# Kernel optimization log

Hardware: AMD Instinct MI355X
Metric: run time of the kernel (lower is better)

Reference implementation:

```python
import jax, jax.numpy as jnp
import numpy as np
from jax import lax

N, R, W, H = 256, 32, 8, 6       # batch, n_rooms, room width/height
MX, MY = 72, 72                  # map grid
EMB = 6                          # room embedding width
CIN = 10 + EMB                   # conv input channels


def _boundaries(m):
    # m: [R, W, H] binary room masks -> [R, 4, W, H] (left, right, up, down edges)
    left = jnp.concatenate([m[:, :1, :], jnp.clip(m[:, 1:, :] - m[:, :-1, :], 0)], axis=1)
    right = jnp.concatenate([jnp.clip(m[:, :-1, :] - m[:, 1:, :], 0), m[:, -1:, :]], axis=1)
    up = jnp.concatenate([m[:, :, :1], jnp.clip(m[:, :, 1:] - m[:, :, :-1], 0)], axis=2)
    down = jnp.concatenate([jnp.clip(m[:, :, :-1] - m[:, :, 1:], 0), m[:, :, -1:]], axis=2)
    return jnp.stack([left, right, up, down], axis=1)


def setup_inputs() -> dict:
    key = jax.random.key(0)
    ks = jax.random.split(key, 12)
    room_map = (jax.random.uniform(ks[0], (R, W, H)) < 0.7).astype(jnp.float32)
    room_map = room_map.at[:, 0, 0].set(1.0)  # guarantee nonempty rooms
    doors = (jax.random.uniform(ks[1], (R, 4, W, H)) < 0.15).astype(jnp.float32) * room_map[:, None]
    room_tensor = jnp.concatenate([room_map[:, None], doors, _boundaries(room_map)], axis=1)  # [R,9,W,H]
    px = jax.random.randint(ks[2], (N, R), 0, MX - W)
    py = jax.random.randint(ks[3], (N, R), 0, MY - H)
    room_positions = jnp.stack([px, py], axis=-1).astype(jnp.int32)  # [N,R,2]

    def rn(k, shape, fan_in):
        return jax.random.normal(k, shape, jnp.float32) / np.float32(np.sqrt(fan_in))

    inp = dict(room_positions=room_positions, room_tensor=room_tensor)
    inp['room_embedding'] = jax.random.normal(ks[4], (R, EMB), jnp.float32)
    inp['w_conv1'] = rn(ks[5], (64, CIN, 5, 5), CIN * 25); inp['b_conv1'] = jnp.zeros((64,), jnp.float32)
    inp['w_conv2'] = rn(ks[6], (64, 64, 3, 3), 64 * 9);    inp['b_conv2'] = jnp.zeros((64,), jnp.float32)
    inp['w_conv3'] = rn(ks[7], (64, 64, 3, 3), 64 * 9);    inp['b_conv3'] = jnp.zeros((64,), jnp.float32)
    inp['w_room1'] = rn(ks[8], (128, 64), 64);   inp['b_room1'] = jnp.zeros((128,), jnp.float32)
    inp['w_room2'] = rn(ks[9], (128, 128), 128); inp['b_room2'] = jnp.zeros((128,), jnp.float32)
    inp['w_fc1'] = rn(ks[10], (256, 128), 128);  inp['b_fc1'] = jnp.zeros((256,), jnp.float32)
    inp['w_fc2'] = rn(ks[11], (256, 256), 256);  inp['b_fc2'] = jnp.zeros((256,), jnp.float32)
    return inp


def _conv2d_relu(x, w, b):
    pad = w.shape[-1] // 2
    y = lax.conv_general_dilated(x, w, (1, 1), [(pad, pad), (pad, pad)],
                                 dimension_numbers=('NCHW', 'OIHW', 'NCHW'))
    return jax.nn.relu(y + b[None, :, None, None])


def _forward(room_positions, room_tensor, room_embedding,
             w_conv1, b_conv1, w_conv2, b_conv2, w_conv3, b_conv3,
             w_room1, b_room1, w_room2, b_room2, w_fc1, b_fc1, w_fc2, b_fc2):
    room_map = room_tensor[:, 0]                      # [R,W,H]
    px = room_positions[..., 0]                       # [N,R]
    py = room_positions[..., 1]
    # ---- encode_map: scatter-add all rooms into grid ----
    bidx = jnp.arange(N)[:, None, None, None, None]
    cidx = jnp.arange(9)[None, None, :, None, None]
    ix = px[:, :, None, None, None] + jnp.arange(W)[None, None, None, :, None]   # [N,R,1,W,1]
    iy = py[:, :, None, None, None] + jnp.arange(H)[None, None, None, None, :]   # [N,R,1,1,H]
    map9 = jnp.zeros((N, 9, MX, MY), jnp.float32).at[bidx, cidx, ix, iy].add(room_tensor[None])
    eidx = jnp.arange(EMB)[None, None, :, None, None]
    evals = room_embedding[:, :, None, None] * room_map[:, None, :, :]           # [R,EMB,W,H]
    embg = jnp.zeros((N, EMB, MX, MY), jnp.float32).at[bidx, eidx, ix, iy].add(evals[None])
    X = jnp.concatenate([map9, jnp.ones((N, 1, MX, MY), jnp.float32), embg], axis=1)  # [N,16,MX,MY]
    # ---- map convs ----
    X = _conv2d_relu(X, w_conv1, b_conv1)
    X = _conv2d_relu(X, w_conv2, b_conv2)
    X = _conv2d_relu(X, w_conv3, b_conv3)
    # ---- decode_map: gather room tiles, masked mean per room ----
    Xt = jnp.transpose(X, (0, 2, 3, 1))                                          # [N,MX,MY,C]
    g = Xt[jnp.arange(N)[:, None, None, None],
           px[:, :, None, None] + jnp.arange(W)[None, None, :, None],
           py[:, :, None, None] + jnp.arange(H)[None, None, None, :]]            # [N,R,W,H,C]
    g = g * room_map[None, :, :, :, None]
    room_feat = g.sum(axis=(2, 3)) / room_map.sum(axis=(1, 2))[None, :, None]    # [N,R,C]
    X = jnp.transpose(room_feat, (0, 2, 1))                                      # [N,C,R]
    # ---- 1x1 conv1d room layers ----
    X = jax.nn.relu(jnp.einsum('ncr,oc->nor', X, w_room1) + b_room1[None, :, None])
    X = jax.nn.relu(jnp.einsum('ncr,oc->nor', X, w_room2) + b_room2[None, :, None])
    # ---- fc head: sum over rooms, MLP ----
    X = X.sum(axis=2)                                                            # [N,128]
    X = jax.nn.relu(X @ w_fc1.T + b_fc1)
    return X @ w_fc2.T + b_fc2                                                   # [N,256]


def reference(room_positions, room_tensor, room_embedding,
              w_conv1, b_conv1, w_conv2, b_conv2, w_conv3, b_conv3,
              w_room1, b_room1, w_room2, b_room2, w_fc1, b_fc1, w_fc2, b_fc2):
    return _forward(room_positions, room_tensor, room_embedding,
                    w_conv1, b_conv1, w_conv2, b_conv2, w_conv3, b_conv3,
                    w_room1, b_room1, w_room2, b_room2, w_fc1, b_fc1, w_fc2, b_fc2)
```

## Files before the change

### kernel.cpp

```cpp
#include <hip/hip_runtime.h>
#include <hip/hip_bf16.h>
#include <cstddef>

#define NB 256
#define RR 32
#define WW 8
#define HH 6
#define MXY 72
#define EMB 6
#define CIN1 16

typedef __bf16 bf16x8 __attribute__((ext_vector_type(8)));
typedef float floatx4 __attribute__((ext_vector_type(4)));

static const size_t B_W1F  = 0;
static const size_t B_W2F  = 57344;
static const size_t B_W3F  = 131072;
static const size_t B_RAUX = 204800;
static const size_t B_RINV = 205056;
static const size_t B_HEAD = 205312;
static const size_t F_WR1T = 0;
static const size_t F_WR2T = 8192;
static const size_t F_F1T  = 24576;
static const size_t F_F2T  = 57344;
static const size_t B_FEAT = 696832;
static const size_t B_CHUNK = 2793984;
static const size_t PERN_BYTES = 165888;

__device__ inline short f2b(float f) {
    unsigned u = __builtin_bit_cast(unsigned, f);
    unsigned r = (u + 0x7fffu + ((u >> 16) & 1u)) >> 16;
    return (short)r;
}

__global__ void prep_weights(const float* __restrict__ w1, const float* __restrict__ w2,
                             const float* __restrict__ w3, const float* __restrict__ wr1,
                             const float* __restrict__ wr2, const float* __restrict__ wf1,
                             const float* __restrict__ wf2, char* __restrict__ ws)
{
    short* W1F = (short*)(ws + B_W1F);
    short* W2F = (short*)(ws + B_W2F);
    short* W3F = (short*)(ws + B_W3F);
    float* HEAD = (float*)(ws + B_HEAD);

    int idx = blockIdx.x * 256 + threadIdx.x;
    if (idx < 28672) {
        int j = idx & 7, lane = (idx >> 3) & 63, nt = (idx >> 9) & 3, kk = idx >> 11;
        int k = kk * 32 + (lane >> 4) * 8 + j;
        int oc = nt * 16 + (lane & 15);
        int tap = k >> 4, ci = k & 15;
        float v = (tap < 25) ? w1[(oc * 16 + ci) * 25 + tap] : 0.f;
        W1F[idx] = f2b(v);
        return;
    }
    idx -= 28672;
    if (idx < 36864) {
        int j = idx & 7, lane = (idx >> 3) & 63, nt = (idx >> 9) & 3, kk = idx >> 11;
        int k = kk * 32 + (lane >> 4) * 8 + j;
        int oc = nt * 16 + (lane & 15);
        int tap = k >> 6, cp = k & 63;
        int ci = (cp >> 2) + (cp & 3) * 16;
        W2F[idx] = f2b(w2[(oc * 64 + ci) * 9 + tap]);
        return;
    }
    idx -= 36864;
    if (idx < 36864) {
        int j = idx & 7, lane = (idx >> 3) & 63, nt = (idx >> 9) & 3, kk = idx >> 11;
        int k = kk * 32 + (lane >> 4) * 8 + j;
        int oc = nt * 16 + (lane & 15);
        int tap = k >> 6, cp = k & 63;
        int ci = (cp >> 2) + (cp & 3) * 16;
        W3F[idx] = f2b(w3[(oc * 64 + ci) * 9 + tap]);
        return;
    }
    idx -= 36864;
    if (idx < 8192)  { int o = idx & 127, c = idx >> 7; HEAD[F_WR1T + idx] = wr1[o * 64 + c]; return; }
    idx -= 8192;
    if (idx < 16384) { int o = idx & 127, c = idx >> 7; HEAD[F_WR2T + idx] = wr2[o * 128 + c]; return; }
    idx -= 16384;
    if (idx < 32768) { int o = idx & 255, c = idx >> 8; HEAD[F_F1T + idx] = wf1[o * 128 + c]; return; }
    idx -= 32768;
    if (idx < 65536) { int o = idx & 255, c = idx >> 8; HEAD[F_F2T + idx] = wf2[o * 256 + c]; return; }
}

__global__ void prep_rooms(const float* __restrict__ rt, char* __restrict__ ws)
{
    int r = threadIdx.x;
    if (r >= RR) return;
    unsigned long long m = 0ull;
    int cnt = 0;
    for (int j = 0; j < WW * HH; ++j)
        if (rt[r * 9 * 48 + j] != 0.f) { m |= (1ull << j); ++cnt; }
    ((unsigned long long*)(ws + B_RAUX))[r] = m;
    ((float*)(ws + B_RINV))[r] = 1.f / (float)cnt;
}

__global__ __launch_bounds__(256) void build_x(const int* __restrict__ pos,
                                               const float* __restrict__ rt,
                                               const float* __restrict__ emb,
                                               short* __restrict__ X, int n0)
{
    const int nl = blockIdx.y;
    const int n = n0 + nl;
    const int p = blockIdx.x * 256 + threadIdx.x;

    __shared__ int s_px[RR], s_py[RR];
    __shared__ float s_emb[RR * EMB];
    if (threadIdx.x < RR) {
        s_px[threadIdx.x] = pos[(n * RR + threadIdx.x) * 2 + 0];
        s_py[threadIdx.x] = pos[(n * RR + threadIdx.x) * 2 + 1];
    }
    for (int i = threadIdx.x; i < RR * EMB; i += 256) s_emb[i] = emb[i];
    __syncthreads();
    if (p >= MXY * MXY) return;

    const int gx = p / MXY, gy = p - (p / MXY) * MXY;

    float acc[16];
#pragma unroll
    for (int c = 0; c < 16; ++c) acc[c] = 0.f;
    acc[9] = 1.f;

    for (int r = 0; r < RR; ++r) {
        int w = gx - s_px[r], h = gy - s_py[r];
        if ((unsigned)w < (unsigned)WW && (unsigned)h < (unsigned)HH) {
            int j = w * HH + h;
            const float* rr = rt + r * 9 * 48;
#pragma unroll
            for (int c = 0; c < 9; ++c) acc[c] += rr[c * 48 + j];
            float m = rr[j];
#pragma unroll
            for (int e = 0; e < EMB; ++e) acc[10 + e] += s_emb[r * EMB + e] * m;
        }
    }

    short o[16];
#pragma unroll
    for (int c = 0; c < 16; ++c) o[c] = f2b(acc[c]);
    short* dst = X + ((size_t)nl * (MXY * MXY) + p) * CIN1;
    *reinterpret_cast<uint4*>(dst) = *reinterpret_cast<uint4*>(o);
    *reinterpret_cast<uint4*>(dst + 8) = *reinterpret_cast<uint4*>(o + 8);
}

__global__ __launch_bounds__(256, 4) void fused_conv(const short* __restrict__ X,
    const short* __restrict__ wAll, const float* __restrict__ bc1,
    const float* __restrict__ bc2, const float* __restrict__ bc3,
    const int* __restrict__ pos, const unsigned long long* __restrict__ rmask,
    float* __restrict__ feat, int n0)
{
    __shared__ __align__(16) short s_Y1[120 * 72];
    __shared__ __align__(16) short s_u[80 * 72];
    __shared__ float s_feat[64];

    const int tid = threadIdx.x;
    const int lane = tid & 63;
    const int wv = tid >> 6;
    const int ml = lane & 15;
    const int q = lane >> 4;
    const int room = blockIdx.x;
    const int nl = blockIdx.y;
    const int n = n0 + nl;

    const int px = pos[(n * RR + room) * 2 + 0];
    const int py = pos[(n * RR + room) * 2 + 1];

    const short* W1F = wAll;
    const short* W2F = wAll + B_W2F / 2;
    const short* W3F = wAll + B_W3F / 2;

    bf16x8 Bb[2][4];
    auto load_k = [&](const short* wF, int kk, bf16x8* dst) {
        const short* src = wF + (size_t)kk * 2048;
#pragma unroll
        for (int j2 = 0; j2 < 4; ++j2)
            dst[j2] = *reinterpret_cast<const bf16x8*>(src + (j2 * 64 + lane) * 8);
    };

    load_k(W1F, 0, Bb[0]);

    const short* Xn = X + (size_t)nl * (MXY * MXY) * CIN1;
    for (int i = tid; i < 448; i += 256) {
        int half = i & 1, pix = i >> 1;
        int row = pix / 14, col = pix - row * 14;
        int gx = px - 4 + row, gy = py - 4 + col;
        uint4 v = make_uint4(0u, 0u, 0u, 0u);
        if ((unsigned)gx < (unsigned)MXY && (unsigned)gy < (unsigned)MXY)
            v = *reinterpret_cast<const uint4*>(Xn + ((size_t)gx * MXY + gy) * CIN1 + half * 8);
        *reinterpret_cast<uint4*>(&s_u[pix * 24 + half * 8]) = v;
    }
    __syncthreads();

    {
        int prow[2], pcol[2];
#pragma unroll
        for (int i = 0; i < 2; ++i) {
            int p = wv * 32 + i * 16 + ml;
            if (p > 119) p = 119;
            prow[i] = p / 10; pcol[i] = p - prow[i] * 10;
        }
        floatx4 acc1[2][4] = {};

#pragma unroll
        for (int kk = 0; kk < 13; ++kk) {
            if (kk < 12) load_k(W1F, kk + 1, Bb[(kk + 1) & 1]);
            else         load_k(W2F, 0, Bb[1]);
            int tap = kk * 2 + (q >> 1);
            if (tap > 24) tap = 24;
            int chb = (q & 1) * 8;
            int dx = tap / 5, dy = tap - dx * 5;
            __builtin_amdgcn_s_setprio(1);
#pragma unroll
            for (int i = 0; i < 2; ++i) {
                bf16x8 A = *reinterpret_cast<const bf16x8*>(
                    &s_u[((prow[i] + dx) * 14 + (pcol[i] + dy)) * 24 + chb]);
#pragma unroll
                for (int j2 = 0; j2 < 4; ++j2)
                    acc1[i][j2] = __builtin_amdgcn_mfma_f32_16x16x32_bf16(
                        A, Bb[kk & 1][j2], acc1[i][j2], 0, 0, 0);
            }
            __builtin_amdgcn_s_setprio(0);
        }
        float b4[4];
#pragma unroll
        for (int j2 = 0; j2 < 4; ++j2) b4[j2] = bc1[j2 * 16 + ml];
#pragma unroll
        for (int i = 0; i < 2; ++i)
#pragma unroll
            for (int r = 0; r < 4; ++r) {
                int p = wv * 32 + i * 16 + q * 4 + r;
                if (p < 120) {
                    unsigned lo = (unsigned)(unsigned short)f2b(fmaxf(acc1[i][0][r] + b4[0], 0.f))
                                | ((unsigned)(unsigned short)f2b(fmaxf(acc1[i][1][r] + b4[1], 0.f)) << 16);
                    unsigned hi = (unsigned)(unsigned short)f2b(fmaxf(acc1[i][2][r] + b4[2], 0.f))
                                | ((unsigned)(unsigned short)f2b(fmaxf(acc1[i][3][r] + b4[3], 0.f)) << 16);
                    *reinterpret_cast<uint2*>(&s_Y1[p * 72 + ml * 4]) = make_uint2(lo, hi);
                }
            }
    }
    __syncthreads();

    {
        int prowA, pcolA, prowB, pcolB;
        {
            int p0 = wv * 16 + ml; prowA = p0 >> 3; pcolA = p0 & 7;
            int p1 = 64 + ml;      prowB = p1 >> 3; pcolB = p1 & 7;
        }
        floatx4 acc2[4] = {};
        floatx4 acc2s = {};

#pragma unroll
        for (int kk = 0; kk < 18; ++kk) {
            if (kk < 17) load_k(W2F, kk + 1, Bb[kk & 1]);
            else         load_k(W3F, 0, Bb[1]);
            bf16x8 B4 = *reinterpret_cast<const bf16x8*>(
                W2F + (size_t)kk * 2048 + (wv * 64 + lane) * 8);
            const int tap = kk >> 1;
            const int chb = (kk & 1) * 32 + q * 8;
            const int dx = tap / 3, dy = tap - (tap / 3) * 3;
            bf16x8 A0 = *reinterpret_cast<const bf16x8*>(
                &s_Y1[((prowA + dx) * 10 + (pcolA + dy)) * 72 + chb]);
            bf16x8 A4 = *reinterpret_cast<const bf16x8*>(
                &s_Y1[((prowB + dx) * 10 + (pcolB + dy)) * 72 + chb]);
            __builtin_amdgcn_s_setprio(1);
#pragma unroll
            for (int j2 = 0; j2 < 4; ++j2)
                acc2[j2] = __builtin_amdgcn_mfma_f32_16x16x32_bf16(A0, Bb[(kk + 1) & 1][j2], acc2[j2], 0, 0, 0);
            acc2s = __builtin_amdgcn_mfma_f32_16x16x32_bf16(A4, B4, acc2s, 0, 0, 0);
            __builtin_amdgcn_s_setprio(0);
        }
        float b4[4];
#pragma unroll
        for (int j2 = 0; j2 < 4; ++j2) b4[j2] = bc2[j2 * 16 + ml];
#pragma unroll
        for (int r = 0; r < 4; ++r) {
            int p = wv * 16 + q * 4 + r;
            unsigned lo = (unsigned)(unsigned short)f2b(fmaxf(acc2[0][r] + b4[0], 0.f))
                        | ((unsigned)(unsigned short)f2b(fmaxf(acc2[1][r] + b4[1], 0.f)) << 16);
            unsigned hi = (unsigned)(unsigned short)f2b(fmaxf(acc2[2][r] + b4[2], 0.f))
                        | ((unsigned)(unsigned short)f2b(fmaxf(acc2[3][r] + b4[3], 0.f)) << 16);
            *reinterpret_cast<uint2*>(&s_u[p * 72 + ml * 4]) = make_uint2(lo, hi);
        }
        {
            float bt = bc2[wv * 16 + ml];
#pragma unroll
            for (int r = 0; r < 4; ++r) {
                int p = 64 + q * 4 + r;
                s_u[p * 72 + ml * 4 + wv] = f2b(fmaxf(acc2s[r] + bt, 0.f));
            }
        }
        if (tid < 64) s_feat[tid] = 0.f;
    }
    __syncthreads();

    if (wv < 3) {
        int p0 = wv * 16 + ml;
        int row3 = p0 / 6, col3 = p0 - (p0 / 6) * 6;
        floatx4 acc3[4] = {};

#pragma unroll
        for (int kk = 0; kk < 18; ++kk) {
            if (kk < 17) load_k(W3F, kk + 1, Bb[kk & 1]);
            const int tap = kk >> 1;
            const int chb = (kk & 1) * 32 + q * 8;
            const int dx = tap / 3, dy = tap - (tap / 3) * 3;
            bf16x8 A = *reinterpret_cast<const bf16x8*>(
                &s_u[((row3 + dx) * 8 + (col3 + dy)) * 72 + chb]);
            __builtin_amdgcn_s_setprio(1);
#pragma unroll
            for (int j2 = 0; j2 < 4; ++j2)
                acc3[j2] = __builtin_amdgcn_mfma_f32_16x16x32_bf16(A, Bb[(kk + 1) & 1][j2], acc3[j2], 0, 0, 0);
            __builtin_amdgcn_s_setprio(0);
        }
        float b4[4];
#pragma unroll
        for (int j2 = 0; j2 < 4; ++j2) b4[j2] = bc3[j2 * 16 + ml];
        float part[4] = {0.f, 0.f, 0.f, 0.f};
        const unsigned long long mk = rmask[room];
#pragma unroll
        for (int r = 0; r < 4; ++r) {
            int p = wv * 16 + q * 4 + r;
            if ((mk >> p) & 1ull) {
#pragma unroll
                for (int j2 = 0; j2 < 4; ++j2)
                    part[j2] += fmaxf(acc3[j2][r] + b4[j2], 0.f);
            }
        }
#pragma unroll
        for (int j2 = 0; j2 < 4; ++j2) {
            part[j2] += __shfl_xor(part[j2], 16);
            part[j2] += __shfl_xor(part[j2], 32);
        }
        if (q == 0) {
#pragma unroll
            for (int j2 = 0; j2 < 4; ++j2)
                atomicAdd(&s_feat[j2 * 16 + ml], part[j2]);
        }
    }
    __syncthreads();
    if (tid < 64)
        feat[((size_t)n * RR + room) * 64 + tid] = s_feat[tid];
}

__global__ __launch_bounds__(256) void mlp_head(const float* __restrict__ feat,
                                                const float* __restrict__ HEAD,
                                                const float* __restrict__ rinv,
                                                const float* __restrict__ b1,
                                                const float* __restrict__ b2,
                                                const float* __restrict__ bf1,
                                                const float* __restrict__ bf2,
                                                float* __restrict__ outp)
{
    __shared__ __align__(16) float s_feat[RR * 64];
    __shared__ __align__(16) float s_h1[RR * 128];
    __shared__ __align__(16) float s_s[2 * 128];
    __shared__ __align__(16) float s_sf[128];
    __shared__ __align__(16) float s_t1[256];

    const int n = blockIdx.x;
    const int tid = threadIdx.x;
    const float* W1t = HEAD + F_WR1T;
    const float* W2t = HEAD + F_WR2T;
    const float* F1t = HEAD + F_F1T;
    const float* F2t = HEAD + F_F2T;

    for (int i = tid; i < RR * 64; i += 256)
        s_feat[i] = feat[(size_t)n * RR * 64 + i] * rinv[i >> 6];
    __syncthreads();

    const int o = tid & 127;
    const int rh = tid >> 7;

    float acc[16];
#pragma unroll
    for (int r = 0; r < 16; ++r) acc[r] = b1[o];
    for (int c4 = 0; c4 < 16; ++c4) {
        float w0 = W1t[(c4 * 4 + 0) * 128 + o];
        float w1 = W1t[(c4 * 4 + 1) * 128 + o];
        float w2 = W1t[(c4 * 4 + 2) * 128 + o];
        float w3 = W1t[(c4 * 4 + 3) * 128 + o];
#pragma unroll
        for (int r = 0; r < 16; ++r) {
            float4 f = *reinterpret_cast<const float4*>(&s_feat[(rh * 16 + r) * 64 + c4 * 4]);
            acc[r] += f.x * w0 + f.y * w1 + f.z * w2 + f.w * w3;
        }
    }
#pragma unroll
    for (int r = 0; r < 16; ++r) s_h1[(rh * 16 + r) * 128 + o] = fmaxf(acc[r], 0.f);
    __syncthreads();

#pragma unroll
    for (int r = 0; r < 16; ++r) acc[r] = b2[o];
    for (int c4 = 0; c4 < 32; ++c4) {
        float w0 = W2t[(c4 * 4 + 0) * 128 + o];
        float w1 = W2t[(c4 * 4 + 1) * 128 + o];
        float w2 = W2t[(c4 * 4 + 2) * 128 + o];
        float w3 = W2t[(c4 * 4 + 3) * 128 + o];
#pragma unroll
        for (int r = 0; r < 16; ++r) {
            float4 f = *reinterpret_cast<const float4*>(&s_h1[(rh * 16 + r) * 128 + c4 * 4]);
            acc[r] += f.x * w0 + f.y * w1 + f.z * w2 + f.w * w3;
        }
    }
    float ps = 0.f;
#pragma unroll
    for (int r = 0; r < 16; ++r) ps += fmaxf(acc[r], 0.f);
    s_s[rh * 128 + o] = ps;
    __syncthreads();
    if (tid < 128) s_sf[tid] = s_s[tid] + s_s[128 + tid];
    __syncthreads();

    {
        float a = bf1[tid];
        for (int c4 = 0; c4 < 32; ++c4) {
            float4 f = *reinterpret_cast<const float4*>(&s_sf[c4 * 4]);
            a += f.x * F1t[(c4 * 4 + 0) * 256 + tid];
            a += f.y * F1t[(c4 * 4 + 1) * 256 + tid];
            a += f.z * F1t[(c4 * 4 + 2) * 256 + tid];
            a += f.w * F1t[(c4 * 4 + 3) * 256 + tid];
        }
        s_t1[tid] = fmaxf(a, 0.f);
    }
    __syncthreads();

    {
        float a = bf2[tid];
        for (int c4 = 0; c4 < 64; ++c4) {
            float4 f = *reinterpret_cast<const float4*>(&s_t1[c4 * 4]);
            a += f.x * F2t[(c4 * 4 + 0) * 256 + tid];
            a += f.y * F2t[(c4 * 4 + 1) * 256 + tid];
            a += f.z * F2t[(c4 * 4 + 2) * 256 + tid];
            a += f.w * F2t[(c4 * 4 + 3) * 256 + tid];
        }
        outp[(size_t)n * 256 + tid] = a;
    }
}

extern "C" void kernel_launch(void* const* d_in, const int* in_sizes, int n_in,
                              void* d_out, int out_size, void* d_ws, size_t ws_size,
                              hipStream_t stream)
{
    const int* pos = (const int*)d_in[0];
    const float* rt = (const float*)d_in[1];
    const float* emb = (const float*)d_in[2];
    const float* w1 = (const float*)d_in[3];
    const float* bc1 = (const float*)d_in[4];
    const float* w2 = (const float*)d_in[5];
    const float* bc2 = (const float*)d_in[6];
    const float* w3 = (const float*)d_in[7];
    const float* bc3 = (const float*)d_in[8];
    const float* wr1 = (const float*)d_in[9];
    const float* br1 = (const float*)d_in[10];
    const float* wr2 = (const float*)d_in[11];
    const float* br2 = (const float*)d_in[12];
    const float* wf1 = (const float*)d_in[13];
    const float* bf1 = (const float*)d_in[14];
    const float* wf2 = (const float*)d_in[15];
    const float* bf2 = (const float*)d_in[16];
    float* out = (float*)d_out;
    char* ws = (char*)d_ws;

    prep_weights<<<880, 256, 0, stream>>>(w1, w2, w3, wr1, wr2, wf1, wf2, ws);
    prep_rooms<<<1, 64, 0, stream>>>(rt, ws);

    int nc = 16;
    const int cands[4] = {256, 128, 64, 32};
    for (int k = 0; k < 4; ++k) {
        size_t need = B_CHUNK + (size_t)cands[k] * PERN_BYTES;
        if (need <= ws_size) { nc = cands[k]; break; }
    }

    const short* WALL = (const short*)(ws + B_W1F);
    const unsigned long long* RMASK = (const unsigned long long*)(ws + B_RAUX);
    const float* RINV = (const float*)(ws + B_RINV);
    float* HEAD = (float*)(ws + B_HEAD);
    float* FEAT = (float*)(ws + B_FEAT);
    short* Xc = (short*)(ws + B_CHUNK);

    for (int n0 = 0; n0 < NB; n0 += nc) {
        build_x<<<dim3(21, nc), 256, 0, stream>>>(pos, rt, emb, Xc, n0);
        fused_conv<<<dim3(RR, nc), 256, 0, stream>>>(Xc, WALL, bc1, bc2, bc3,
                                                     pos, RMASK, FEAT, n0);
    }

    mlp_head<<<NB, 256, 0, stream>>>(FEAT, HEAD, RINV, br1, br2, bf1, bf2, out);
}
```

Baseline: 331.1 us.

## Fuse map construction into conv kernel using per-room overlap masks

Removes the separate build_x pass that rasterized the full 72x72x16 map for every batch element into a global buffer. Each conv block now builds only its own 14x16 patch, and a new prep kernel computes per-room bitmasks of nearby rooms so only candidate rooms are tested. The chunked batch loop is replaced by a single launch. This avoids the global write and read of the intermediate map at the cost of redundant rasterization in overlapping patches and uncoalesced global loads inside the conv kernel prologue.

```diff
diff --git a/kernel.cpp b/kernel.cpp
--- a/kernel.cpp
+++ b/kernel.cpp
@@ -24,8 +24,7 @@
 static const size_t F_F1T  = 24576;
 static const size_t F_F2T  = 57344;
 static const size_t B_FEAT = 696832;
-static const size_t B_CHUNK = 2793984;
-static const size_t PERN_BYTES = 165888;
+static const size_t B_IMSK = 2793984;
 
 __device__ inline short f2b(float f) {
     unsigned u = __builtin_bit_cast(unsigned, f);
@@ -95,58 +94,28 @@
     ((float*)(ws + B_RINV))[r] = 1.f / (float)cnt;
 }
 
-__global__ __launch_bounds__(256) void build_x(const int* __restrict__ pos,
-                                               const float* __restrict__ rt,
-                                               const float* __restrict__ emb,
-                                               short* __restrict__ X, int n0)
-{
-    const int nl = blockIdx.y;
-    const int n = n0 + nl;
-    const int p = blockIdx.x * 256 + threadIdx.x;
-
-    __shared__ int s_px[RR], s_py[RR];
-    __shared__ float s_emb[RR * EMB];
-    if (threadIdx.x < RR) {
-        s_px[threadIdx.x] = pos[(n * RR + threadIdx.x) * 2 + 0];
-        s_py[threadIdx.x] = pos[(n * RR + threadIdx.x) * 2 + 1];
-    }
-    for (int i = threadIdx.x; i < RR * EMB; i += 256) s_emb[i] = emb[i];
-    __syncthreads();
-    if (p >= MXY * MXY) return;
-
-    const int gx = p / MXY, gy = p - (p / MXY) * MXY;
-
-    float acc[16];
-#pragma unroll
-    for (int c = 0; c < 16; ++c) acc[c] = 0.f;
-    acc[9] = 1.f;
-
+__global__ void prep_imask(const int* __restrict__ pos, unsigned* __restrict__ imask)
+{
+    const int n = blockIdx.x;
+    const int r0 = threadIdx.x;
+    const int px0 = pos[(n * RR + r0) * 2 + 0];
+    const int py0 = pos[(n * RR + r0) * 2 + 1];
+    unsigned m = 0;
     for (int r = 0; r < RR; ++r) {
-        int w = gx - s_px[r], h = gy - s_py[r];
-        if ((unsigned)w < (unsigned)WW && (unsigned)h < (unsigned)HH) {
-            int j = w * HH + h;
-            const float* rr = rt + r * 9 * 48;
-#pragma unroll
-            for (int c = 0; c < 9; ++c) acc[c] += rr[c * 48 + j];
-            float m = rr[j];
-#pragma unroll
-            for (int e = 0; e < EMB; ++e) acc[10 + e] += s_emb[r * EMB + e] * m;
-        }
-    }
-
-    short o[16];
-#pragma unroll
-    for (int c = 0; c < 16; ++c) o[c] = f2b(acc[c]);
-    short* dst = X + ((size_t)nl * (MXY * MXY) + p) * CIN1;
-    *reinterpret_cast<uint4*>(dst) = *reinterpret_cast<uint4*>(o);
-    *reinterpret_cast<uint4*>(dst + 8) = *reinterpret_cast<uint4*>(o + 8);
-}
-
-__global__ __launch_bounds__(256, 4) void fused_conv(const short* __restrict__ X,
-    const short* __restrict__ wAll, const float* __restrict__ bc1,
-    const float* __restrict__ bc2, const float* __restrict__ bc3,
-    const int* __restrict__ pos, const unsigned long long* __restrict__ rmask,
-    float* __restrict__ feat, int n0)
+        int rpx = pos[(n * RR + r) * 2 + 0];
+        int rpy = pos[(n * RR + r) * 2 + 1];
+        if (rpx >= px0 - 11 && rpx <= px0 + 11 && rpy >= py0 - 9 && rpy <= py0 + 9)
+            m |= 1u << r;
+    }
+    imask[n * RR + r0] = m;
+}
+
+__global__ __launch_bounds__(256, 4) void fused_conv(
+    const unsigned* __restrict__ imask, const float* __restrict__ rt,
+    const float* __restrict__ emb, const short* __restrict__ wAll,
+    const float* __restrict__ bc1, const float* __restrict__ bc2,
+    const float* __restrict__ bc3, const int* __restrict__ pos,
+    const unsigned long long* __restrict__ rmask, float* __restrict__ feat)
 {
     __shared__ __align__(16) short s_Y1[120 * 72];
     __shared__ __align__(16) short s_u[80 * 72];
@@ -158,8 +127,7 @@
     const int ml = lane & 15;
     const int q = lane >> 4;
     const int room = blockIdx.x;
-    const int nl = blockIdx.y;
-    const int n = n0 + nl;
+    const int n = blockIdx.y;
 
     const int px = pos[(n * RR + room) * 2 + 0];
     const int py = pos[(n * RR + room) * 2 + 1];
@@ -178,15 +146,39 @@
 
     load_k(W1F, 0, Bb[0]);
 
-    const short* Xn = X + (size_t)nl * (MXY * MXY) * CIN1;
-    for (int i = tid; i < 448; i += 256) {
-        int half = i & 1, pix = i >> 1;
-        int row = pix / 14, col = pix - row * 14;
-        int gx = px - 4 + row, gy = py - 4 + col;
-        uint4 v = make_uint4(0u, 0u, 0u, 0u);
-        if ((unsigned)gx < (unsigned)MXY && (unsigned)gy < (unsigned)MXY)
-            v = *reinterpret_cast<const uint4*>(Xn + ((size_t)gx * MXY + gy) * CIN1 + half * 8);
-        *reinterpret_cast<uint4*>(&s_u[pix * 24 + half * 8]) = v;
+    {
+        const unsigned mk0 = imask[n * RR + room];
+        if (tid < 224) {
+            const int row = tid / 14, col = tid - (tid / 14) * 14;
+            const int gx = px - 4 + row, gy = py - 4 + col;
+            float a[16];
+#pragma unroll
+            for (int c = 0; c < 16; ++c) a[c] = 0.f;
+            a[9] = ((unsigned)gx < (unsigned)MXY && (unsigned)gy < (unsigned)MXY) ? 1.f : 0.f;
+
+            unsigned mm = mk0;
+            while (mm) {
+                const int r = __builtin_ctz(mm);
+                mm &= mm - 1;
+                const int rpx = pos[(n * RR + r) * 2 + 0];
+                const int rpy = pos[(n * RR + r) * 2 + 1];
+                const int w = gx - rpx, h = gy - rpy;
+                if ((unsigned)w < (unsigned)WW && (unsigned)h < (unsigned)HH) {
+                    const int j = w * HH + h;
+                    const float* rr = rt + r * 9 * 48;
+#pragma unroll
+                    for (int c = 0; c < 9; ++c) a[c] += rr[c * 48 + j];
+                    const float mv = rr[j];
+#pragma unroll
+                    for (int e = 0; e < EMB; ++e) a[10 + e] += emb[r * EMB + e] * mv;
+                }
+            }
+            short o[16];
+#pragma unroll
+            for (int c = 0; c < 16; ++c) o[c] = f2b(a[c]);
+            *reinterpret_cast<uint4*>(&s_u[tid * 24 + 0]) = *reinterpret_cast<uint4*>(o);
+            *reinterpret_cast<uint4*>(&s_u[tid * 24 + 8]) = *reinterpret_cast<uint4*>(o + 8);
+        }
     }
     __syncthreads();
 
@@ -462,25 +454,17 @@
     prep_weights<<<880, 256, 0, stream>>>(w1, w2, w3, wr1, wr2, wf1, wf2, ws);
     prep_rooms<<<1, 64, 0, stream>>>(rt, ws);
 
-    int nc = 16;
-    const int cands[4] = {256, 128, 64, 32};
-    for (int k = 0; k < 4; ++k) {
-        size_t need = B_CHUNK + (size_t)cands[k] * PERN_BYTES;
-        if (need <= ws_size) { nc = cands[k]; break; }
-    }
-
     const short* WALL = (const short*)(ws + B_W1F);
     const unsigned long long* RMASK = (const unsigned long long*)(ws + B_RAUX);
     const float* RINV = (const float*)(ws + B_RINV);
     float* HEAD = (float*)(ws + B_HEAD);
     float* FEAT = (float*)(ws + B_FEAT);
-    short* Xc = (short*)(ws + B_CHUNK);
-
-    for (int n0 = 0; n0 < NB; n0 += nc) {
-        build_x<<<dim3(21, nc), 256, 0, stream>>>(pos, rt, emb, Xc, n0);
-        fused_conv<<<dim3(RR, nc), 256, 0, stream>>>(Xc, WALL, bc1, bc2, bc3,
-                                                     pos, RMASK, FEAT, n0);
-    }
+    unsigned* IMSK = (unsigned*)(ws + B_IMSK);
+
+    prep_imask<<<NB, RR, 0, stream>>>(pos, IMSK);
+
+    fused_conv<<<dim3(RR, NB), 256, 0, stream>>>(IMSK, rt, emb, WALL,
+                                                 bc1, bc2, bc3, pos, RMASK, FEAT);
 
     mlp_head<<<NB, 256, 0, stream>>>(FEAT, HEAD, RINV, br1, br2, bf1, bf2, out);
 }
```

Result: faster. 312.1 us (-5.7%).
